# Optimization experiments

Measured on AMD Instinct MI355X. Metric: run time of the kernel, lower is better.

## Reference

```python
import jax, jax.numpy as jnp
import numpy as np

# Pangu-Weather EarthAttention3D, dim=192 branch
H = 6                 # heads
D = 192               # dim
DH = D // H           # head dim = 32
N = 2 * 6 * 12        # window tokens = 144
TW = (8 // 2) * (186 // 6)  # type_of_windows = 124
NW = 8                # number of windows (leading batch axis)
SCALE = DH ** -0.5


def setup_inputs() -> dict:
    key = jax.random.key(0)
    ks = jax.random.split(key, 7)
    return {
        "x": jax.random.normal(ks[0], (NW, TW, N, D), jnp.float32),
        "mask": jax.random.normal(ks[1], (NW, TW, N, N), jnp.float32),
        "w_qkv": jax.random.normal(ks[2], (D, 3 * D), jnp.float32) * 0.02,
        "b_qkv": jnp.zeros((3 * D,), jnp.float32),
        "bias": jax.random.normal(ks[3], (1, TW, H, N, N), jnp.float32) * 0.02,
        "w_out": jax.random.normal(ks[4], (D, D), jnp.float32) * 0.02,
        "b_out": jnp.zeros((D,), jnp.float32),
    }


def reference(x, mask, w_qkv, b_qkv, bias, w_out, b_out):
    B, W, Ntok, Dm = x.shape  # (nW, type_of_windows, win_tokens, dim)
    # fused QKV projection
    qkv = (x @ w_qkv + b_qkv).reshape(B, W, Ntok, 3, H, DH)
    qkv = jnp.transpose(qkv, (3, 0, 1, 4, 2, 5))  # (3, B, W, H, N, dh)
    q, k, v = qkv[0] * SCALE, qkv[1], qkv[2]
    # scores + earth-specific bias + window mask (broadcast over heads)
    attn = jnp.einsum('bwhnd,bwhmd->bwhnm', q, k)
    attn = attn + bias + mask[:, :, None, :, :]
    attn = jax.nn.softmax(attn, axis=-1)  # dropout_rate=0 -> identity
    out = jnp.einsum('bwhnm,bwhmd->bwhnd', attn, v)
    out = jnp.transpose(out, (0, 1, 3, 2, 4)).reshape(B, W, Ntok, Dm)
    return out @ w_out + b_out
```

## Files before the change

### kernel.cpp

```cpp
#include <hip/hip_runtime.h>
#include <hip/hip_bf16.h>

typedef __bf16 bf16_t;
typedef bf16_t bf16x8 __attribute__((ext_vector_type(8)));
typedef bf16_t bf16x4 __attribute__((ext_vector_type(4)));
typedef float f32x4 __attribute__((ext_vector_type(4)));

#define SCALE 0.17677669529663687f

#define PIN(x) asm volatile("" : "+v"(x))

__device__ __forceinline__ int swz_elem(int r, int c) {
    int g = c >> 3;
    return r * 192 + ((g >> 3) << 6) + (((g & 7) ^ (r & 7)) << 3) + (c & 7);
}

__device__ __forceinline__ void stage_chunk(bf16_t* dst, const bf16_t* src, int tid) {
#pragma unroll
    for (int it = 0; it < 3; ++it) {
        int off = (it * 256 + tid) * 8;
        __builtin_amdgcn_global_load_lds(
            (const __attribute__((address_space(1))) unsigned int*)(src + off),
            (__attribute__((address_space(3))) unsigned int*)(dst + off),
            16, 0, 0);
    }
}

__device__ __forceinline__ void stage_1k(bf16_t* dst, const bf16_t* src, int lane) {
    __builtin_amdgcn_global_load_lds(
        (const __attribute__((address_space(1))) unsigned int*)(src + lane * 8),
        (__attribute__((address_space(3))) unsigned int*)(dst + lane * 8),
        16, 0, 0);
}

__global__ void prep_weights(const float* __restrict__ w_qkv, const float* __restrict__ w_out,
                             bf16_t* __restrict__ wqkvS, bf16_t* __restrict__ woutS) {
    int i = blockIdx.x * 256 + threadIdx.x;
    if (i < 576 * 192) {
        int o = i / 192, k = i % 192;
        float v = w_qkv[k * 576 + o];
        if (o < 192) v *= SCALE;
        wqkvS[(o >> 5) * 6144 + swz_elem(o & 31, k)] = (bf16_t)v;
    }
    if (i < 192 * 192) {
        int o = i / 192, k = i % 192;
        woutS[(o >> 5) * 6144 + swz_elem(o & 31, k)] = (bf16_t)w_out[k * 192 + o];
    }
}

__global__ __launch_bounds__(256, 8)
void prep_bm2(const float* __restrict__ bias, const float* __restrict__ mask,
              bf16_t* __restrict__ biasP, bf16_t* __restrict__ maskP)
{
    __shared__ bf16_t L[16 * 148];
    int blk = blockIdx.x;
    bool isMask = blk >= 6696;
    int region = isMask ? blk - 6696 : blk;
    int rg = region / 9, t = region % 9;
    const float* src = (isMask ? mask : bias) + ((size_t)rg * 144 + t * 16) * 144;
    bf16_t* dst = (isMask ? maskP : biasP) + (size_t)region * 2560;
    const int tid = threadIdx.x;

    for (int i = tid; i < 576; i += 256) {
        int row = i / 36, seg = i % 36;
        f32x4 v = *(const f32x4*)(src + row * 144 + seg * 4);
        bf16x4 o;
        o[0] = (bf16_t)v[0]; o[1] = (bf16_t)v[1]; o[2] = (bf16_t)v[2]; o[3] = (bf16_t)v[3];
        *(bf16x4*)&L[row * 148 + seg * 4] = o;
    }
    __syncthreads();

    for (int u = tid; u < 320; u += 256) {
        int it = u >> 6, lane = u & 63;
        int lrow = lane & 15, lgrp = lane >> 4;
        bf16x8 o;
#pragma unroll
        for (int e = 0; e < 8; ++e) {
            int us = it * 8 + e;
            int nt = us >> 2, j = us & 3;
            int m = (us < 36) ? (nt * 16 + lgrp * 4 + j) : 0;
            bf16_t v = L[lrow * 148 + m];
            o[e] = (us < 36) ? v : (bf16_t)0.f;
        }
        *(bf16x8*)(dst + it * 512 + lane * 8) = o;
    }
}

__global__ __launch_bounds__(256, 5)
void qkv_gemm(const float* __restrict__ x, const float* __restrict__ b_qkv,
              const bf16_t* __restrict__ wqkvS,
              bf16_t* __restrict__ Qg, bf16_t* __restrict__ Kg, bf16_t* __restrict__ Vt)
{
    __shared__ __align__(16) bf16_t Wb[2][6144];
    __shared__ __align__(16) bf16_t T[4][640];
    __shared__ float bl[192];
    const int tid  = threadIdx.x;
    const int lane = tid & 63;
    const int wave = tid >> 6;
    const int lrow = lane & 15;
    const int lgrp = lane >> 4;
    const int m    = blockIdx.x / 3;
    const int kind = blockIdx.x % 3;
    const int r0   = m * 64 + wave * 16;
    const int c0   = m % 6;

    if (tid < 192) bl[tid] = b_qkv[kind * 192 + tid];

    const bf16_t* wbase = wqkvS + kind * 6 * 6144;
    stage_chunk(&Wb[0][0], wbase + c0 * 6144, tid);

    bf16x8 af[6];
#pragma unroll
    for (int ks = 0; ks < 6; ++ks) {
        const float* px = x + (size_t)(r0 + lrow) * 192 + ks * 32 + lgrp * 8;
        f32x4 lo = *(const f32x4*)px;
        f32x4 hi = *(const f32x4*)(px + 4);
        bf16x8 v;
        v[0] = (bf16_t)lo[0]; v[1] = (bf16_t)lo[1]; v[2] = (bf16_t)lo[2]; v[3] = (bf16_t)lo[3];
        v[4] = (bf16_t)hi[0]; v[5] = (bf16_t)hi[1]; v[6] = (bf16_t)hi[2]; v[7] = (bf16_t)hi[3];
        af[ks] = v;
    }
    __syncthreads();

    bf16_t* tl = &T[wave][0];

#pragma unroll 1
    for (int i = 0; i < 6; ++i) {
        int h = c0 + i; if (h >= 6) h -= 6;

        if (i < 5) {
            int nc = c0 + i + 1; if (nc >= 6) nc -= 6;
            stage_chunk(&Wb[(i + 1) & 1][0], wbase + nc * 6144, tid);
        }
        const bf16_t* wb = &Wb[i & 1][0];

        f32x4 a0{0.f, 0.f, 0.f, 0.f}, a1{0.f, 0.f, 0.f, 0.f};
#pragma unroll
        for (int ks = 0; ks < 6; ++ks) {
            bf16x8 wf0 = *(const bf16x8*)&wb[swz_elem(lrow,      ks * 32 + lgrp * 8)];
            bf16x8 wf1 = *(const bf16x8*)&wb[swz_elem(16 + lrow, ks * 32 + lgrp * 8)];
            a0 = __builtin_amdgcn_mfma_f32_16x16x32_bf16(af[ks], wf0, a0, 0, 0, 0);
            a1 = __builtin_amdgcn_mfma_f32_16x16x32_bf16(af[ks], wf1, a1, 0, 0, 0);
        }

        float b0 = bl[h * 32 + lrow], b1 = bl[h * 32 + 16 + lrow];
        if (kind == 0) { b0 *= SCALE; b1 *= SCALE; }

        if (kind < 2) {
            bf16_t* dst = (kind == 0) ? Qg : Kg;
#pragma unroll
            for (int j = 0; j < 4; ++j) {
                tl[(lgrp * 4 + j) * 40 + lrow]      = (bf16_t)(a0[j] + b0);
                tl[(lgrp * 4 + j) * 40 + 16 + lrow] = (bf16_t)(a1[j] + b1);
            }
            bf16x8 val = *(const bf16x8*)&tl[lrow * 40 + lgrp * 8];
            int tk = r0 + lrow, bw = tk / 144, n = tk % 144;
            *(bf16x8*)&dst[((size_t)(bw * 6 + h) * 144 + n) * 32 + lgrp * 8] = val;
        } else {
#pragma unroll
            for (int j = 0; j < 4; ++j) {
                tl[(lrow) * 20      + lgrp * 4 + j] = (bf16_t)(a0[j] + b0);
                tl[(16 + lrow) * 20 + lgrp * 4 + j] = (bf16_t)(a1[j] + b1);
            }
            int d = lane >> 1, cg = lane & 1;
            int tk = r0 + cg * 8, bw = tk / 144, n = tk % 144;
            bf16x8 val = *(const bf16x8*)&tl[d * 20 + cg * 8];
            *(bf16x8*)&Vt[((size_t)(bw * 6 + h) * 32 + d) * 160 + n] = val;
        }

        if (i < 5) {
            asm volatile("s_waitcnt vmcnt(1)" ::: "memory");
            __builtin_amdgcn_sched_barrier(0);
            __builtin_amdgcn_s_barrier();
            __builtin_amdgcn_sched_barrier(0);
        }
    }
}

__global__ __launch_bounds__(192, 3)
void earth_attn_v10(const bf16_t* __restrict__ Qg, const bf16_t* __restrict__ Kg,
                    const bf16_t* __restrict__ Vt,
                    const bf16_t* __restrict__ maskP, const bf16_t* __restrict__ biasP,
                    bf16_t* __restrict__ Og)
{
    __shared__ __align__(16) bf16_t Kl[4608];
    __shared__ __align__(16) bf16_t Vl[5120];
    __shared__ __align__(16) bf16_t P[3][16 * 168];
    const int tid  = threadIdx.x;
    const int lane = tid & 63;
    const int wave = tid >> 6;
    const int lrow = lane & 15;
    const int lgrp = lane >> 4;

    const int orig = blockIdx.x;
    const int blk  = (orig & 7) * 744 + (orig >> 3);

    const int ww = blk / 48;
    const int r1 = blk % 48;
    const int b  = r1 / 6;
    const int h  = r1 % 6;
    const int bw = b * 124 + ww;

    const size_t kbase = ((size_t)(bw * 6 + h) * 144) * 32;
    const size_t vbase = ((size_t)(bw * 6 + h) * 32) * 160;

    for (int c = wave; c < 9; c += 3)  stage_1k(Kl + c * 512, Kg + kbase + c * 512, lane);
    for (int c = wave; c < 10; c += 3) stage_1k(Vl + c * 512, Vt + vbase + c * 512, lane);

    bf16_t* pb = &P[wave][0];
    {
        uint2 z2 = make_uint2(0u, 0u);
        *(uint2*)&pb[lrow * 168 + 144 + lgrp * 4] = z2;
    }
    __syncthreads();

    const bf16_t* bpB = biasP + (size_t)(ww * 6 + h) * 9 * 2560 + lane * 8;
    const bf16_t* mpB = maskP + (size_t)bw * 9 * 2560 + lane * 8;
    bf16_t* ogp = Og + ((size_t)bw * 144) * 192 + h * 32 + lgrp * 8;

#pragma unroll 1
    for (int i = 0; i < 3; ++i) {
        const int t = wave + i * 3;

        bf16x8 bvv[5], mvv[5];
#pragma unroll
        for (int it = 0; it < 5; ++it) {
            bvv[it] = *(const bf16x8*)(bpB + (size_t)t * 2560 + it * 512);
            mvv[it] = *(const bf16x8*)(mpB + (size_t)t * 2560 + it * 512);
        }
        bf16x8 qa = *(const bf16x8*)&Qg[kbase + (size_t)(t * 16 + lrow) * 32 + lgrp * 8];

        f32x4 s[9];
#pragma unroll
        for (int nt = 0; nt < 9; ++nt)
#pragma unroll
            for (int j = 0; j < 4; ++j) {
                const int u = nt * 4 + j;
                s[nt][j] = (float)bvv[u >> 3][u & 7] + (float)mvv[u >> 3][u & 7];
            }

#pragma unroll
        for (int nt = 0; nt < 9; ++nt) {
            bf16x8 ka = *(const bf16x8*)&Kl[(nt * 16 + lrow) * 32 + lgrp * 8];
            s[nt] = __builtin_amdgcn_mfma_f32_16x16x32_bf16(ka, qa, s[nt], 0, 0, 0);
        }

        float mx = -1e30f;
#pragma unroll
        for (int nt = 0; nt < 9; ++nt)
#pragma unroll
            for (int j = 0; j < 4; ++j) mx = fmaxf(mx, s[nt][j]);
        mx = fmaxf(mx, __shfl_xor(mx, 16, 64));
        mx = fmaxf(mx, __shfl_xor(mx, 32, 64));
        float sum = 0.f;
#pragma unroll
        for (int nt = 0; nt < 9; ++nt)
#pragma unroll
            for (int j = 0; j < 4; ++j) { float e = __expf(s[nt][j] - mx); s[nt][j] = e; sum += e; }
        sum += __shfl_xor(sum, 16, 64);
        sum += __shfl_xor(sum, 32, 64);
        const float rinv = 1.0f / sum;

#pragma unroll
        for (int nt = 0; nt < 9; ++nt) {
            bf16x4 pw;
#pragma unroll
            for (int j = 0; j < 4; ++j) pw[j] = (bf16_t)(s[nt][j] * rinv);
            *(bf16x4*)&pb[lrow * 168 + nt * 16 + lgrp * 4] = pw;
        }

        f32x4 o0{0.f, 0.f, 0.f, 0.f}, o1{0.f, 0.f, 0.f, 0.f};
#pragma unroll
        for (int ks = 0; ks < 5; ++ks) {
            bf16x8 pa = *(const bf16x8*)&pb[lrow * 168 + ks * 32 + lgrp * 8];
            bf16x8 v0 = *(const bf16x8*)&Vl[lrow * 160 + ks * 32 + lgrp * 8];
            bf16x8 v1 = *(const bf16x8*)&Vl[(16 + lrow) * 160 + ks * 32 + lgrp * 8];
            o0 = __builtin_amdgcn_mfma_f32_16x16x32_bf16(pa, v0, o0, 0, 0, 0);
            o1 = __builtin_amdgcn_mfma_f32_16x16x32_bf16(pa, v1, o1, 0, 0, 0);
        }

#pragma unroll
        for (int j = 0; j < 4; ++j) {
            pb[(lgrp * 4 + j) * 168 + lrow]      = (bf16_t)o0[j];
            pb[(lgrp * 4 + j) * 168 + 16 + lrow] = (bf16_t)o1[j];
        }
        bf16x8 ov = *(const bf16x8*)&pb[lrow * 168 + lgrp * 8];
        *(bf16x8*)(ogp + (size_t)(t * 16 + lrow) * 192) = ov;
    }
}

__global__ __launch_bounds__(256, 2)
void earth_attn_v7(const bf16_t* __restrict__ Qg, const bf16_t* __restrict__ Kg,
                   const bf16_t* __restrict__ Vt,
                   const float* __restrict__ mask, const float* __restrict__ bias,
                   bf16_t* __restrict__ Og)
{
    __shared__ bf16_t P[4][16 * 168];
    const int tid  = threadIdx.x;
    const int lane = tid & 63;
    const int wave = tid >> 6;
    const int lrow = lane & 15;
    const int lgrp = lane >> 4;
    const int orig = blockIdx.x;
    const int blk  = (orig & 7) * 186 + (orig >> 3);
    const int wid = blk * 4 + wave;
    const int ww  = wid / 48;
    const int r1  = wid % 48;
    const int b   = r1 / 6;
    const int h   = r1 % 6;
    const int bw  = b * 124 + ww;
    const size_t kbase = ((size_t)(bw * 6 + h) * 144) * 32;
    const size_t vbase = ((size_t)(bw * 6 + h) * 32) * 160;

    bf16x8 ka[9];
#pragma unroll
    for (int nt = 0; nt < 9; ++nt)
        ka[nt] = *(const bf16x8*)&Kg[kbase + (size_t)(nt * 16 + lrow) * 32 + lgrp * 8];
    bf16x8 va0[5], va1[5];
#pragma unroll
    for (int ks = 0; ks < 5; ++ks) {
        va0[ks] = *(const bf16x8*)&Vt[vbase + (size_t)lrow * 160 + ks * 32 + lgrp * 8];
        va1[ks] = *(const bf16x8*)&Vt[vbase + (size_t)(16 + lrow) * 160 + ks * 32 + lgrp * 8];
    }
    const float* bp_base = bias + (size_t)(ww * 6 + h) * 144 * 144;
    const float* mp_base = mask + (size_t)bw * 144 * 144;
    bf16_t* pb = &P[wave][0];
    bf16_t* ogp = Og + ((size_t)bw * 144) * 192 + h * 32 + lgrp * 8;
    bf16x8 qa = *(const bf16x8*)&Qg[kbase + (size_t)lrow * 32 + lgrp * 8];
    f32x4 bv[9], mv[9];
    {
        const float* bp = bp_base + (size_t)lrow * 144;
        const float* mp = mp_base + (size_t)lrow * 144;
#pragma unroll
        for (int nt = 0; nt < 9; ++nt) {
            bv[nt] = *(const f32x4*)(bp + nt * 16 + lgrp * 4);
            mv[nt] = *(const f32x4*)(mp + nt * 16 + lgrp * 4);
        }
    }
#pragma unroll 1
    for (int t = 0; t < 9; ++t) {
        f32x4 s[9];
#pragma unroll
        for (int nt = 0; nt < 9; ++nt) s[nt] = bv[nt] + mv[nt];
        const int tn = (t < 8) ? t + 1 : 8;
        bf16x8 qa_n = *(const bf16x8*)&Qg[kbase + (size_t)(tn * 16 + lrow) * 32 + lgrp * 8];
        {
            const float* bp = bp_base + (size_t)(tn * 16 + lrow) * 144;
            const float* mp = mp_base + (size_t)(tn * 16 + lrow) * 144;
#pragma unroll
            for (int nt = 0; nt < 9; ++nt) {
                bv[nt] = *(const f32x4*)(bp + nt * 16 + lgrp * 4);
                mv[nt] = *(const f32x4*)(mp + nt * 16 + lgrp * 4);
            }
        }
#pragma unroll
        for (int nt = 0; nt < 9; ++nt)
            s[nt] = __builtin_amdgcn_mfma_f32_16x16x32_bf16(ka[nt], qa, s[nt], 0, 0, 0);
        float mx = -1e30f;
#pragma unroll
        for (int nt = 0; nt < 9; ++nt)
#pragma unroll
            for (int j = 0; j < 4; ++j) mx = fmaxf(mx, s[nt][j]);
        mx = fmaxf(mx, __shfl_xor(mx, 16, 64));
        mx = fmaxf(mx, __shfl_xor(mx, 32, 64));
        float sum = 0.f;
#pragma unroll
        for (int nt = 0; nt < 9; ++nt)
#pragma unroll
            for (int j = 0; j < 4; ++j) { float e = __expf(s[nt][j] - mx); s[nt][j] = e; sum += e; }
        sum += __shfl_xor(sum, 16, 64);
        sum += __shfl_xor(sum, 32, 64);
        const float rinv = 1.0f / sum;
#pragma unroll
        for (int nt = 0; nt < 9; ++nt) {
            bf16x4 pw;
#pragma unroll
            for (int j = 0; j < 4; ++j) pw[j] = (bf16_t)(s[nt][j] * rinv);
            *(bf16x4*)&pb[lrow * 168 + nt * 16 + lgrp * 4] = pw;
        }
        {
            uint2 z2 = make_uint2(0u, 0u);
            *(uint2*)&pb[lrow * 168 + 144 + lgrp * 4] = z2;
        }
        bf16x8 pa[5];
#pragma unroll
        for (int ks = 0; ks < 5; ++ks)
            pa[ks] = *(const bf16x8*)&pb[lrow * 168 + ks * 32 + lgrp * 8];
#pragma unroll
        for (int ks = 0; ks < 5; ++ks) PIN(pa[ks]);
        f32x4 o0{0.f, 0.f, 0.f, 0.f}, o1{0.f, 0.f, 0.f, 0.f};
#pragma unroll
        for (int ks = 0; ks < 5; ++ks) {
            o0 = __builtin_amdgcn_mfma_f32_16x16x32_bf16(pa[ks], va0[ks], o0, 0, 0, 0);
            o1 = __builtin_amdgcn_mfma_f32_16x16x32_bf16(pa[ks], va1[ks], o1, 0, 0, 0);
        }
#pragma unroll
        for (int j = 0; j < 4; ++j) {
            pb[(lgrp * 4 + j) * 168 + lrow]      = (bf16_t)o0[j];
            pb[(lgrp * 4 + j) * 168 + 16 + lrow] = (bf16_t)o1[j];
        }
        bf16x8 ov = *(const bf16x8*)&pb[lrow * 168 + lgrp * 8];
        *(bf16x8*)(ogp + (size_t)(t * 16 + lrow) * 192) = ov;
        qa = qa_n;
    }
}

__global__ __launch_bounds__(256, 4)
void out_proj(const bf16_t* __restrict__ Og, const bf16_t* __restrict__ woutS,
              const float* __restrict__ b_out, float* __restrict__ out)
{
    __shared__ __align__(16) bf16_t Wb[2][6144];
    const int tid  = threadIdx.x;
    const int lane = tid & 63;
    const int wave = tid >> 6;
    const int lrow = lane & 15;
    const int lgrp = lane >> 4;
    const size_t row0 = (size_t)blockIdx.x * 64 + wave * 16;
    const int c0   = blockIdx.x % 6;

    stage_chunk(&Wb[0][0], woutS + c0 * 6144, tid);

    bf16x8 af[6];
#pragma unroll
    for (int ks = 0; ks < 6; ++ks)
        af[ks] = *(const bf16x8*)(Og + (row0 + lrow) * 192 + ks * 32 + lgrp * 8);
    __syncthreads();

#pragma unroll 1
    for (int i = 0; i < 6; ++i) {
        int c = c0 + i; if (c >= 6) c -= 6;
        if (i < 5) {
            int nc = c + 1; if (nc >= 6) nc -= 6;
            stage_chunk(&Wb[(i + 1) & 1][0], woutS + nc * 6144, tid);
        }
        const bf16_t* wb = &Wb[i & 1][0];
        float b0 = b_out[c * 32 + lrow], b1 = b_out[c * 32 + 16 + lrow];
        f32x4 a0{b0, b0, b0, b0}, a1{b1, b1, b1, b1};
#pragma unroll
        for (int ks = 0; ks < 6; ++ks) {
            bf16x8 wf0 = *(const bf16x8*)&wb[swz_elem(lrow,      ks * 32 + lgrp * 8)];
            bf16x8 wf1 = *(const bf16x8*)&wb[swz_elem(16 + lrow, ks * 32 + lgrp * 8)];
            a0 = __builtin_amdgcn_mfma_f32_16x16x32_bf16(af[ks], wf0, a0, 0, 0, 0);
            a1 = __builtin_amdgcn_mfma_f32_16x16x32_bf16(af[ks], wf1, a1, 0, 0, 0);
        }
        __syncthreads();
#pragma unroll
        for (int j = 0; j < 4; ++j) {
            out[(row0 + lgrp * 4 + j) * 192 + c * 32 + lrow]      = a0[j];
            out[(row0 + lgrp * 4 + j) * 192 + c * 32 + 16 + lrow] = a1[j];
        }
    }
}

extern "C" void kernel_launch(void* const* d_in, const int* in_sizes, int n_in,
                              void* d_out, int out_size, void* d_ws, size_t ws_size,
                              hipStream_t stream) {
    const float* x     = (const float*)d_in[0];
    const float* mask  = (const float*)d_in[1];
    const float* w_qkv = (const float*)d_in[2];
    const float* b_qkv = (const float*)d_in[3];
    const float* bias  = (const float*)d_in[4];
    const float* w_out = (const float*)d_in[5];
    const float* b_out = (const float*)d_in[6];

    bf16_t* wqkvS = (bf16_t*)d_ws;
    bf16_t* woutS = wqkvS + 576 * 192;
    bf16_t* Qg    = woutS + 192 * 192;
    bf16_t* Kg    = Qg + (size_t)992 * 6 * 144 * 32;
    bf16_t* Vt    = Kg + (size_t)992 * 6 * 144 * 32;
    bf16_t* Og    = Vt + (size_t)992 * 6 * 32 * 160;
    bf16_t* biasP = Og + (size_t)992 * 144 * 192;
    bf16_t* maskP = biasP + (size_t)6696 * 2560;

    const size_t need_v10 = ((size_t)112902144 + 17141760 + 22855680) * 2;

    prep_weights<<<dim3(432), dim3(256), 0, stream>>>(w_qkv, w_out, wqkvS, woutS);
    qkv_gemm<<<dim3(6696), dim3(256), 0, stream>>>(x, b_qkv, wqkvS, Qg, Kg, Vt);

    if (ws_size >= need_v10) {
        prep_bm2<<<dim3(15624), dim3(256), 0, stream>>>(bias, mask, biasP, maskP);
        earth_attn_v10<<<dim3(5952), dim3(192), 0, stream>>>(Qg, Kg, Vt, maskP, biasP, Og);
    } else {
        earth_attn_v7<<<dim3(1488), dim3(256), 0, stream>>>(Qg, Kg, Vt, mask, bias, Og);
    }
    out_proj<<<dim3(2232), dim3(256), 0, stream>>>(Og, woutS, b_out, (float*)d_out);
}
```

Measured before the change: 275.8 us.

## Compute all QKV columns per row block with register-prefetched weights

Each QKV GEMM block now covers all 18 column chunks for its 64-row tile instead of splitting Q/K/V across three blocks. The converted x fragments are loaded once rather than three times, and blocks drop from 6696 to 2232. Weight fragments are read straight from global memory into double-buffered registers, replacing the LDS staging and the per-chunk barriers, and the bias is read directly from global. Register pressure rises, so launch bounds drop to 3 blocks per CU, and weights are now fetched once per wave rather than once per block.

```diff
diff --git a/kernel.cpp b/kernel.cpp
--- a/kernel.cpp
+++ b/kernel.cpp
@@ -86,28 +86,33 @@
     }
 }
 
-__global__ __launch_bounds__(256, 5)
+#define LOADW(W, cbase)                                                        \
+    {                                                                          \
+        const bf16_t* _c = (cbase);                                            \
+        _Pragma("unroll")                                                      \
+        for (int _ks = 0; _ks < 6; ++_ks) {                                    \
+            W[2 * _ks]     = *(const bf16x8*)&_c[swz_elem(lrow,      _ks * 32 + lgrp * 8)]; \
+            W[2 * _ks + 1] = *(const bf16x8*)&_c[swz_elem(16 + lrow, _ks * 32 + lgrp * 8)]; \
+        }                                                                      \
+    }
+#define PIN12(W) { _Pragma("unroll") for (int _p = 0; _p < 12; ++_p) PIN(W[_p]); }
+
+__global__ __launch_bounds__(256, 3)
 void qkv_gemm(const float* __restrict__ x, const float* __restrict__ b_qkv,
               const bf16_t* __restrict__ wqkvS,
               bf16_t* __restrict__ Qg, bf16_t* __restrict__ Kg, bf16_t* __restrict__ Vt)
 {
-    __shared__ __align__(16) bf16_t Wb[2][6144];
     __shared__ __align__(16) bf16_t T[4][640];
-    __shared__ float bl[192];
     const int tid  = threadIdx.x;
     const int lane = tid & 63;
     const int wave = tid >> 6;
     const int lrow = lane & 15;
     const int lgrp = lane >> 4;
-    const int m    = blockIdx.x / 3;
-    const int kind = blockIdx.x % 3;
-    const int r0   = m * 64 + wave * 16;
-    const int c0   = m % 6;
-
-    if (tid < 192) bl[tid] = b_qkv[kind * 192 + tid];
-
-    const bf16_t* wbase = wqkvS + kind * 6 * 6144;
-    stage_chunk(&Wb[0][0], wbase + c0 * 6144, tid);
+    const int r0   = blockIdx.x * 64 + wave * 16;
+
+    bf16x8 wA[12], wB[12];
+    LOADW(wA, wqkvS);
+    LOADW(wB, wqkvS + 6144);
 
     bf16x8 af[6];
 #pragma unroll
@@ -120,59 +125,64 @@
         v[4] = (bf16_t)hi[0]; v[5] = (bf16_t)hi[1]; v[6] = (bf16_t)hi[2]; v[7] = (bf16_t)hi[3];
         af[ks] = v;
     }
-    __syncthreads();
+    PIN12(wA);
 
     bf16_t* tl = &T[wave][0];
+    const int tk = r0 + lrow, bwq = tk / 144, nq = tk % 144;
 
 #pragma unroll 1
-    for (int i = 0; i < 6; ++i) {
-        int h = c0 + i; if (h >= 6) h -= 6;
-
-        if (i < 5) {
-            int nc = c0 + i + 1; if (nc >= 6) nc -= 6;
-            stage_chunk(&Wb[(i + 1) & 1][0], wbase + nc * 6144, tid);
-        }
-        const bf16_t* wb = &Wb[i & 1][0];
-
-        f32x4 a0{0.f, 0.f, 0.f, 0.f}, a1{0.f, 0.f, 0.f, 0.f};
-#pragma unroll
-        for (int ks = 0; ks < 6; ++ks) {
-            bf16x8 wf0 = *(const bf16x8*)&wb[swz_elem(lrow,      ks * 32 + lgrp * 8)];
-            bf16x8 wf1 = *(const bf16x8*)&wb[swz_elem(16 + lrow, ks * 32 + lgrp * 8)];
-            a0 = __builtin_amdgcn_mfma_f32_16x16x32_bf16(af[ks], wf0, a0, 0, 0, 0);
-            a1 = __builtin_amdgcn_mfma_f32_16x16x32_bf16(af[ks], wf1, a1, 0, 0, 0);
-        }
-
-        float b0 = bl[h * 32 + lrow], b1 = bl[h * 32 + 16 + lrow];
-        if (kind == 0) { b0 *= SCALE; b1 *= SCALE; }
-
-        if (kind < 2) {
-            bf16_t* dst = (kind == 0) ? Qg : Kg;
-#pragma unroll
-            for (int j = 0; j < 4; ++j) {
-                tl[(lgrp * 4 + j) * 40 + lrow]      = (bf16_t)(a0[j] + b0);
-                tl[(lgrp * 4 + j) * 40 + 16 + lrow] = (bf16_t)(a1[j] + b1);
+    for (int ii = 0; ii < 9; ++ii) {
+#pragma unroll
+        for (int half = 0; half < 2; ++half) {
+            const int hc = 2 * ii + half;
+            const int kind = hc / 6, h = hc - kind * 6;
+
+            f32x4 a0{0.f, 0.f, 0.f, 0.f}, a1{0.f, 0.f, 0.f, 0.f};
+            if (half == 0) {
+#pragma unroll
+                for (int ks = 0; ks < 6; ++ks) {
+                    a0 = __builtin_amdgcn_mfma_f32_16x16x32_bf16(af[ks], wA[2 * ks],     a0, 0, 0, 0);
+                    a1 = __builtin_amdgcn_mfma_f32_16x16x32_bf16(af[ks], wA[2 * ks + 1], a1, 0, 0, 0);
+                }
+            } else {
+#pragma unroll
+                for (int ks = 0; ks < 6; ++ks) {
+                    a0 = __builtin_amdgcn_mfma_f32_16x16x32_bf16(af[ks], wB[2 * ks],     a0, 0, 0, 0);
+                    a1 = __builtin_amdgcn_mfma_f32_16x16x32_bf16(af[ks], wB[2 * ks + 1], a1, 0, 0, 0);
+                }
             }
-            bf16x8 val = *(const bf16x8*)&tl[lrow * 40 + lgrp * 8];
-            int tk = r0 + lrow, bw = tk / 144, n = tk % 144;
-            *(bf16x8*)&dst[((size_t)(bw * 6 + h) * 144 + n) * 32 + lgrp * 8] = val;
-        } else {
-#pragma unroll
-            for (int j = 0; j < 4; ++j) {
-                tl[(lrow) * 20      + lgrp * 4 + j] = (bf16_t)(a0[j] + b0);
-                tl[(16 + lrow) * 20 + lgrp * 4 + j] = (bf16_t)(a1[j] + b1);
+
+            float b0 = b_qkv[hc * 32 + lrow], b1 = b_qkv[hc * 32 + 16 + lrow];
+            if (kind == 0) { b0 *= SCALE; b1 *= SCALE; }
+
+            if (kind < 2) {
+                bf16_t* dst = (kind == 0) ? Qg : Kg;
+#pragma unroll
+                for (int j = 0; j < 4; ++j) {
+                    tl[(lgrp * 4 + j) * 40 + lrow]      = (bf16_t)(a0[j] + b0);
+                    tl[(lgrp * 4 + j) * 40 + 16 + lrow] = (bf16_t)(a1[j] + b1);
+                }
+                bf16x8 val = *(const bf16x8*)&tl[lrow * 40 + lgrp * 8];
+                *(bf16x8*)&dst[((size_t)(bwq * 6 + h) * 144 + nq) * 32 + lgrp * 8] = val;
+            } else {
+#pragma unroll
+                for (int j = 0; j < 4; ++j) {
+                    tl[(lrow) * 20      + lgrp * 4 + j] = (bf16_t)(a0[j] + b0);
+                    tl[(16 + lrow) * 20 + lgrp * 4 + j] = (bf16_t)(a1[j] + b1);
+                }
+                int d = lane >> 1, cg = lane & 1;
+                int tk2 = r0 + cg * 8, bw2 = tk2 / 144, n2 = tk2 % 144;
+                bf16x8 val = *(const bf16x8*)&tl[d * 20 + cg * 8];
+                *(bf16x8*)&Vt[((size_t)(bw2 * 6 + h) * 32 + d) * 160 + n2] = val;
             }
-            int d = lane >> 1, cg = lane & 1;
-            int tk = r0 + cg * 8, bw = tk / 144, n = tk % 144;
-            bf16x8 val = *(const bf16x8*)&tl[d * 20 + cg * 8];
-            *(bf16x8*)&Vt[((size_t)(bw * 6 + h) * 32 + d) * 160 + n] = val;
-        }
-
-        if (i < 5) {
-            asm volatile("s_waitcnt vmcnt(1)" ::: "memory");
-            __builtin_amdgcn_sched_barrier(0);
-            __builtin_amdgcn_s_barrier();
-            __builtin_amdgcn_sched_barrier(0);
+
+            if (half == 0) {
+                if (hc + 2 < 18) LOADW(wA, wqkvS + (hc + 2) * 6144);
+                PIN12(wB);
+            } else {
+                if (hc + 2 < 18) LOADW(wB, wqkvS + (hc + 2) * 6144);
+                if (hc + 1 < 18) PIN12(wA);
+            }
         }
     }
 }
@@ -475,7 +485,7 @@
     const size_t need_v10 = ((size_t)112902144 + 17141760 + 22855680) * 2;
 
     prep_weights<<<dim3(432), dim3(256), 0, stream>>>(w_qkv, w_out, wqkvS, woutS);
-    qkv_gemm<<<dim3(6696), dim3(256), 0, stream>>>(x, b_qkv, wqkvS, Qg, Kg, Vt);
+    qkv_gemm<<<dim3(2232), dim3(256), 0, stream>>>(x, b_qkv, wqkvS, Qg, Kg, Vt);
 
     if (ws_size >= need_v10) {
         prep_bm2<<<dim3(15624), dim3(256), 0, stream>>>(bias, mask, biasP, maskP);
```

Result: slower. 646.7 us (+134.4%).
